# Optimization experiments

Hardware: AMD Instinct MI355X
Metric: run time of the kernel (lower is better)

## Reference

```python
import jax, jax.numpy as jnp
import numpy as np

NUM_CLASSES = 8
SMOOTH = 1e-05


def setup_inputs() -> dict:
    key = jax.random.key(0)
    k1, k2 = jax.random.split(key)
    inp = jax.random.randint(k1, (8, 512, 512), 0, NUM_CLASSES, dtype=jnp.int64)
    tgt = jax.random.randint(k2, (8, 512, 512), 0, NUM_CLASSES, dtype=jnp.int64)
    weights = jnp.ones((NUM_CLASSES,), dtype=jnp.float32)
    return {"input": inp, "target": tgt, "weights": weights}


def _one_hot_flat(labels):
    # labels: (N, H, W) int -> (N, C, H*W) float32 one-hot
    N = labels.shape[0]
    flat = labels.reshape(N, -1)  # (N, P)
    classes = jnp.arange(NUM_CLASSES)
    return (flat[:, None, :] == classes[None, :, None]).astype(jnp.float32)


def reference(input, target, weights):
    N = input.shape[0]
    oh_in = _one_hot_flat(input)   # (N, C, P)
    oh_tg = _one_hot_flat(target)  # (N, C, P)
    # Dice per class: per-sample intersection and sums over pixels
    inter = jnp.sum(oh_in * oh_tg, axis=-1)            # (N, C)
    sums = jnp.sum(oh_in, axis=-1) + jnp.sum(oh_tg, axis=-1)  # (N, C)
    dice = (2.0 * inter + SMOOTH) / (sums + SMOOTH)    # (N, C)
    each_class_dice = jnp.mean(dice, axis=0)           # (C,) == Dice() per class
    total_loss = jnp.sum(weights * each_class_dice)
    return total_loss, each_class_dice
```

## Files before the change

### kernel.cpp

```cpp
#include <hip/hip_runtime.h>
#include <stdint.h>


#define NCLS   8
#define NSAMP  8
#define PIX    (512 * 512)
#define SMOOTHF 1e-5f

typedef unsigned long long u64;
typedef unsigned int u32;


__global__ __launch_bounds__(256) void dice_count(const int* __restrict__ in,
                                                  const int* __restrict__ tg,
                                                  u32* __restrict__ cnt) {
    const int n = blockIdx.y;
    const int t = threadIdx.x;
    const int4* in4 = (const int4*)(in + (size_t)n * PIX);
    const int4* tg4 = (const int4*)(tg + (size_t)n * PIX);
    const int base = blockIdx.x * 1024;

    u64 pin = 0, ptg = 0, pix = 0;
#pragma unroll
    for (int i = 0; i < 4; ++i) {
        int4 a = in4[base + i * 256 + t];
        int4 b = tg4[base + i * 256 + t];
        u64 ax = 1ull << (a.x * 8), ay = 1ull << (a.y * 8);
        u64 az = 1ull << (a.z * 8), aw = 1ull << (a.w * 8);
        pin += ax + ay + az + aw;
        ptg += (1ull << (b.x * 8)) + (1ull << (b.y * 8)) +
               (1ull << (b.z * 8)) + (1ull << (b.w * 8));
        if (a.x == b.x) pix += ax;
        if (a.y == b.y) pix += ay;
        if (a.z == b.z) pix += az;
        if (a.w == b.w) pix += aw;
    }

    const u64 M = 0x00FF00FF00FF00FFull;
    u64 v[6];
    v[0] = pin & M;
    v[1] = (pin >> 8) & M;
    v[2] = ptg & M;
    v[3] = (ptg >> 8) & M;
    v[4] = pix & M;
    v[5] = (pix >> 8) & M;

#pragma unroll
    for (int off = 1; off < 64; off <<= 1) {
#pragma unroll
        for (int j = 0; j < 6; ++j)
            v[j] += (u64)__shfl_xor((unsigned long long)v[j], off, 64);
    }

    const int lane = t & 63;
    if (lane < 24) {
        const int set = lane >> 3;
        const int c   = lane & 7;
        u64 pk = v[set * 2 + (c & 1)];
        u32 val = (u32)((pk >> (16 * (c >> 1))) & 0xFFFFull);
        atomicAdd(&cnt[n * 24 + set * 8 + c], val);
    }
}

__global__ __launch_bounds__(64) void dice_final(const u32* __restrict__ cnt,
                                                 const float* __restrict__ w,
                                                 float* __restrict__ out) {
    const int lane = threadIdx.x;
    const int n = lane >> 3;
    const int c = lane & 7;
    float cin = (float)cnt[n * 24 + 0 + c];
    float ctg = (float)cnt[n * 24 + 8 + c];
    float itr = (float)cnt[n * 24 + 16 + c];
    float dice = (2.0f * itr + SMOOTHF) / (cin + ctg + SMOOTHF);

    dice += __shfl_xor(dice, 8, 64);
    dice += __shfl_xor(dice, 16, 64);
    dice += __shfl_xor(dice, 32, 64);
    float mean_c = dice * 0.125f;

    if (lane < 8) out[1 + lane] = mean_c;

    float ws = w[c] * mean_c;
    ws += __shfl_xor(ws, 1, 64);
    ws += __shfl_xor(ws, 2, 64);
    ws += __shfl_xor(ws, 4, 64);
    if (lane == 0) out[0] = ws;
}

extern "C" void kernel_launch(void* const* d_in, const int* in_sizes, int n_in,
                              void* d_out, int out_size, void* d_ws, size_t ws_size,
                              hipStream_t stream) {
    const int*   in  = (const int*)d_in[0];
    const int*   tg  = (const int*)d_in[1];
    const float* w   = (const float*)d_in[2];
    float*       out = (float*)d_out;
    u32*         cnt = (u32*)d_ws;

    hipMemsetAsync(d_ws, 0, NSAMP * 24 * sizeof(u32), stream);

    dice_count<<<dim3(64, NSAMP), 256, 0, stream>>>(in, tg, cnt);
    dice_final<<<1, 64, 0, stream>>>(cnt, w, out);
}
```

Before: 81.71 us.

## Replace global atomics and memset with per-block partials and shared-memory reduction

```diff
diff --git a/kernel.cpp b/kernel.cpp
--- a/kernel.cpp
+++ b/kernel.cpp
@@ -2,9 +2,10 @@
 #include <stdint.h>
 
 
-#define NCLS   8
-#define NSAMP  8
-#define PIX    (512 * 512)
+#define NCLS    8
+#define NSAMP   8
+#define PIX     (512 * 512)
+#define BLKS    64
 #define SMOOTHF 1e-5f
 
 typedef unsigned long long u64;
@@ -13,7 +14,7 @@
 
 __global__ __launch_bounds__(256) void dice_count(const int* __restrict__ in,
                                                   const int* __restrict__ tg,
-                                                  u32* __restrict__ cnt) {
+                                                  u32* __restrict__ partial) {
     const int n = blockIdx.y;
     const int t = threadIdx.x;
     const int4* in4 = (const int4*)(in + (size_t)n * PIX);
@@ -36,6 +37,13 @@
         if (a.w == b.w) pix += aw;
     }
 
+#pragma unroll
+    for (int off = 1; off <= 4; off <<= 1) {
+        pin += (u64)__shfl_xor((unsigned long long)pin, off, 64);
+        ptg += (u64)__shfl_xor((unsigned long long)ptg, off, 64);
+        pix += (u64)__shfl_xor((unsigned long long)pix, off, 64);
+    }
+
     const u64 M = 0x00FF00FF00FF00FFull;
     u64 v[6];
     v[0] = pin & M;
@@ -46,45 +54,64 @@
     v[5] = (pix >> 8) & M;
 
 #pragma unroll
-    for (int off = 1; off < 64; off <<= 1) {
+    for (int off = 8; off <= 32; off <<= 1) {
 #pragma unroll
         for (int j = 0; j < 6; ++j)
             v[j] += (u64)__shfl_xor((unsigned long long)v[j], off, 64);
     }
 
+    __shared__ u32 sm[4 * 24];
+    const int wave = t >> 6;
     const int lane = t & 63;
     if (lane < 24) {
         const int set = lane >> 3;
         const int c   = lane & 7;
         u64 pk = v[set * 2 + (c & 1)];
-        u32 val = (u32)((pk >> (16 * (c >> 1))) & 0xFFFFull);
-        atomicAdd(&cnt[n * 24 + set * 8 + c], val);
+        sm[wave * 24 + lane] = (u32)((pk >> (16 * (c >> 1))) & 0xFFFFull);
+    }
+    __syncthreads();
+    if (t < 24) {
+        u32 s = sm[t] + sm[24 + t] + sm[48 + t] + sm[72 + t];
+        partial[((size_t)(n * BLKS + blockIdx.x)) * 24 + t] = s;
     }
 }
 
-__global__ __launch_bounds__(64) void dice_final(const u32* __restrict__ cnt,
-                                                 const float* __restrict__ w,
-                                                 float* __restrict__ out) {
-    const int lane = threadIdx.x;
-    const int n = lane >> 3;
-    const int c = lane & 7;
-    float cin = (float)cnt[n * 24 + 0 + c];
-    float ctg = (float)cnt[n * 24 + 8 + c];
-    float itr = (float)cnt[n * 24 + 16 + c];
-    float dice = (2.0f * itr + SMOOTHF) / (cin + ctg + SMOOTHF);
+__global__ __launch_bounds__(192) void dice_final(const u32* __restrict__ partial,
+                                                  const float* __restrict__ w,
+                                                  float* __restrict__ out) {
+    const int t = threadIdx.x;
+    __shared__ u32 cnt[NSAMP * 24];
 
-    dice += __shfl_xor(dice, 8, 64);
-    dice += __shfl_xor(dice, 16, 64);
-    dice += __shfl_xor(dice, 32, 64);
-    float mean_c = dice * 0.125f;
+    const int n = t / 24;
+    const int i = t - n * 24;
+    u32 s = 0;
+#pragma unroll 8
+    for (int b = 0; b < BLKS; ++b)
+        s += partial[((size_t)(n * BLKS + b)) * 24 + i];
+    cnt[n * 24 + i] = s;
+    __syncthreads();
 
-    if (lane < 8) out[1 + lane] = mean_c;
+    if (t < 64) {
+        const int sn = t >> 3;
+        const int c  = t & 7;
+        float cin = (float)cnt[sn * 24 + 0 + c];
+        float ctg = (float)cnt[sn * 24 + 8 + c];
+        float itr = (float)cnt[sn * 24 + 16 + c];
+        float dice = (2.0f * itr + SMOOTHF) / (cin + ctg + SMOOTHF);
 
-    float ws = w[c] * mean_c;
-    ws += __shfl_xor(ws, 1, 64);
-    ws += __shfl_xor(ws, 2, 64);
-    ws += __shfl_xor(ws, 4, 64);
-    if (lane == 0) out[0] = ws;
+        dice += __shfl_xor(dice, 8, 64);
+        dice += __shfl_xor(dice, 16, 64);
+        dice += __shfl_xor(dice, 32, 64);
+        float mean_c = dice * 0.125f;
+
+        if (t < 8) out[1 + t] = mean_c;
+
+        float ws = w[c] * mean_c;
+        ws += __shfl_xor(ws, 1, 64);
+        ws += __shfl_xor(ws, 2, 64);
+        ws += __shfl_xor(ws, 4, 64);
+        if (t == 0) out[0] = ws;
+    }
 }
 
 extern "C" void kernel_launch(void* const* d_in, const int* in_sizes, int n_in,
@@ -94,10 +121,8 @@
     const int*   tg  = (const int*)d_in[1];
     const float* w   = (const float*)d_in[2];
     float*       out = (float*)d_out;
-    u32*         cnt = (u32*)d_ws;
+    u32*         partial = (u32*)d_ws;
 
-    hipMemsetAsync(d_ws, 0, NSAMP * 24 * sizeof(u32), stream);
-
-    dice_count<<<dim3(64, NSAMP), 256, 0, stream>>>(in, tg, cnt);
-    dice_final<<<1, 64, 0, stream>>>(cnt, w, out);
+    dice_count<<<dim3(BLKS, NSAMP), 256, 0, stream>>>(in, tg, partial);
+    dice_final<<<1, 192, 0, stream>>>(partial, w, out);
 }
```

New measurement: 74.01 us (median of 2 runs). -9.4%, faster.
